# Performance work log

Hardware: AMD Instinct MI355X
Metric: run time of the kernel (lower is better)

The kernel has to match this reference:

```python
import jax, jax.numpy as jnp
import numpy as np

B, L, H, E, EH = 8, 96, 8, 64, 128

def setup_inputs() -> dict:
    key = jax.random.key(0)
    ks = jax.random.split(key, 5)
    x = jax.random.normal(ks[0], (B, L, H, E), jnp.float32)
    # strictly increasing, distinct time points (required by the past/future split)
    gaps = jax.random.uniform(ks[1], (L,), jnp.float32, 0.01, 0.1)
    timeslot = jnp.cumsum(gaps)
    W1 = jax.random.normal(ks[2], (E, EH), jnp.float32) / np.sqrt(E).astype(np.float32)
    b1 = jnp.zeros((EH,), jnp.float32)
    W2 = jax.random.normal(ks[3], (EH, E), jnp.float32) / np.sqrt(EH).astype(np.float32)
    b2 = jnp.zeros((E,), jnp.float32)
    return dict(x=x, timeslot=timeslot, W1=W1, b1=b1, W2=W2, b2=b2)

def reference(x, timeslot, W1, b1, W2, b2):
    Bd, Ld, Hd, Ed = x.shape

    def f(t, y):  # neural odefunc: MLP over feature dim E (t unused by the MLP)
        return jnp.tanh(y @ W1 + b1) @ W2 + b2

    def rk4_step(y, t0, dt):  # torchdiffeq 'rk4' = 3/8-rule RK4, one step per grid interval
        k1 = f(t0, y)
        k2 = f(t0 + dt / 3, y + dt * k1 / 3)
        k3 = f(t0 + 2 * dt / 3, y + dt * (k2 - k1 / 3))
        k4 = f(t0 + dt, y + dt * (k1 - k2 + k3))
        return y + dt * (k1 + 3 * (k2 + k3) + k4) / 8

    # Per-index initial states: S0[idx] = x[:, idx] flattened to (B*H, E)
    S0 = jnp.transpose(x, (1, 0, 2, 3)).reshape(Ld, Bd * Hd, Ed)
    idxs = jnp.arange(Ld)

    # Forward integration: state for index idx is advanced over t_s -> t_{s+1} once s >= idx.
    def fwd_step(S, s):
        t0 = timeslot[s]
        dt = timeslot[s + 1] - t0
        S2 = rk4_step(S, t0, dt)
        S = jnp.where((idxs <= s)[:, None, None], S2, S)
        return S, S  # emitted state corresponds to time t_{s+1}

    _, ys_f = jax.lax.scan(fwd_step, S0, jnp.arange(Ld - 1))
    z_fwd = jnp.concatenate([S0[None], ys_f], axis=0)  # [L_j, L_idx, B*H, E]

    # Backward integration: state for idx is advanced over t_s -> t_{s-1} once s <= idx.
    def bwd_step(S, s):
        t0 = timeslot[s]
        dt = timeslot[s - 1] - t0  # negative
        S2 = rk4_step(S, t0, dt)
        S = jnp.where((idxs >= s)[:, None, None], S2, S)
        return S, S  # emitted state corresponds to time t_{s-1}

    _, ys_b = jax.lax.scan(bwd_step, S0, jnp.arange(Ld - 1, 0, -1))
    z_bwd = jnp.concatenate([jnp.flip(ys_b, axis=0), S0[None]], axis=0)  # [L_j, L_idx, B*H, E]

    jj = jnp.arange(Ld)[:, None]
    z = jnp.where((jj >= idxs[None, :])[:, :, None, None], z_fwd, z_bwd)
    z = z.reshape(Ld, Ld, Bd, Hd, Ed)          # [L_j, L_idx, B, H, E]
    x1 = jnp.transpose(z, (2, 1, 0, 3, 4))      # [B, L_idx, L_j, H, E]
    x0 = jnp.broadcast_to(x[:, :, None], (Bd, Ld, Ld, Hd, Ed))
    return jnp.stack([x0, x1], axis=-1)          # [B, L, L, H, E, 2]
```

## Files before the change

kernel.cpp:

```cpp
#include <hip/hip_runtime.h>
#include <stdint.h>

#define Lc 96
#define Hc 8
#define Ec 64
#define EHc 128
#define APu 72
#define HPu 136
#define JS (Hc * Ec * 2)

typedef __attribute__((ext_vector_type(8))) short short8;
typedef __attribute__((ext_vector_type(4))) float floatx4;

union FragH { uint16_t h[8]; short8 v; };

__device__ __forceinline__ float fast_tanh(float x) {
    const float e = __builtin_amdgcn_exp2f(x * 2.8853900817779268f);
    return 1.0f - 2.0f * __builtin_amdgcn_rcpf(e + 1.0f);
}

__device__ __forceinline__ void lds_barrier() {
    asm volatile("s_waitcnt lgkmcnt(0)\n\ts_barrier" ::: "memory");
}

__global__ __launch_bounds__(256, 2)
void ode_mfma_kernel(const float* __restrict__ x, const float* __restrict__ ts,
                     const float* __restrict__ W1, const float* __restrict__ b1,
                     const float* __restrict__ W2, const float* __restrict__ b2,
                     float* __restrict__ out)
{
    __shared__ alignas(16) uint16_t A_hi[16 * APu];
    __shared__ alignas(16) uint16_t A_lo[16 * APu];
    __shared__ alignas(16) uint16_t H_hi[16 * HPu];
    __shared__ alignas(16) uint16_t H_lo[16 * HPu];
    __shared__ float tss[Lc];

    const int tid  = threadIdx.x;
    const int w    = tid >> 6;
    const int lane = tid & 63;
    const int g    = lane >> 4;
    const int c    = lane & 15;

    if (tid < Lc) tss[tid] = ts[tid];

    short8 w1h[2][2], w1l[2][2];
#pragma unroll
    for (int ct = 0; ct < 2; ++ct)
#pragma unroll
        for (int ks = 0; ks < 2; ++ks) {
            FragH fh, fl;
#pragma unroll
            for (int j = 0; j < 8; ++j) {
                const int k = ks * 32 + g * 8 + j;
                const int n = 32 * w + 16 * ct + c;
                const float v = W1[k * EHc + n];
                const uint32_t uv = __float_as_uint(v);
                const float hf = __uint_as_float(uv & 0xffff0000u);
                fh.h[j] = (uint16_t)(uv >> 16);
                fl.h[j] = (uint16_t)(__float_as_uint(v - hf) >> 16);
            }
            w1h[ct][ks] = fh.v; w1l[ct][ks] = fl.v;
        }
    short8 w2h[4], w2l[4];
#pragma unroll
    for (int ks = 0; ks < 4; ++ks) {
        FragH fh, fl;
#pragma unroll
        for (int j = 0; j < 8; ++j) {
            const int k = ks * 32 + g * 8 + j;
            const int n = 16 * w + c;
            const float v = W2[k * Ec + n];
            const uint32_t uv = __float_as_uint(v);
            const float hf = __uint_as_float(uv & 0xffff0000u);
            fh.h[j] = (uint16_t)(uv >> 16);
            fl.h[j] = (uint16_t)(__float_as_uint(v - hf) >> 16);
        }
        w2h[ks] = fh.v; w2l[ks] = fl.v;
    }

    const float b1v0 = b1[32 * w + c];
    const float b1v1 = b1[32 * w + 16 + c];
    const float b2v  = b2[16 * w + c];

    const int t_blk = (blockIdx.x * 16) >> 6;
    const int fs    = (Lc - 1) - t_blk;
    const int col   = 16 * w + c;

    float y0_[4], y_[4];
    float* outp[4];
#pragma unroll
    for (int reg = 0; reg < 4; ++reg) {
        const int rs = blockIdx.x * 16 + g * 4 + reg;
        const int bidx = (rs & 63) >> 3;
        const int hh   = rs & 7;
        const float v0 = x[((bidx * Lc + t_blk) * Hc + hh) * Ec + col];
        y0_[reg] = v0; y_[reg] = v0;
        outp[reg] = out + (size_t)(bidx * Lc + t_blk) * (Lc * JS) + hh * (Ec * 2) + col * 2;
        float2 o; o.x = v0; o.y = v0;
        *(float2*)(outp[reg] + (size_t)t_blk * JS) = o;
        const int r = g * 4 + reg;
        const uint32_t uv = __float_as_uint(v0);
        A_hi[r * APu + col] = (uint16_t)(uv >> 16);
        A_lo[r * APu + col] =
            (uint16_t)(__float_as_uint(v0 - __uint_as_float(uv & 0xffff0000u)) >> 16);
    }
    __syncthreads();

    const int arow = c * APu + g * 8;
    const int hrow = c * HPu + g * 8;
    const int hcol = 32 * w + c;

    auto evalf = [&]() -> floatx4 {
        const short8 a0h = *(const short8*)(A_hi + arow);
        const short8 a1h = *(const short8*)(A_hi + arow + 32);
        const short8 a0l = *(const short8*)(A_lo + arow);
        const short8 a1l = *(const short8*)(A_lo + arow + 32);

        floatx4 p0 = {b1v0, b1v0, b1v0, b1v0};
        floatx4 p1 = {b1v1, b1v1, b1v1, b1v1};
        p0 = __builtin_amdgcn_mfma_f32_16x16x32_bf16(a0h, w1h[0][0], p0, 0, 0, 0);
        p0 = __builtin_amdgcn_mfma_f32_16x16x32_bf16(a0h, w1l[0][0], p0, 0, 0, 0);
        p0 = __builtin_amdgcn_mfma_f32_16x16x32_bf16(a0l, w1h[0][0], p0, 0, 0, 0);
        p1 = __builtin_amdgcn_mfma_f32_16x16x32_bf16(a0h, w1h[1][0], p1, 0, 0, 0);
        p1 = __builtin_amdgcn_mfma_f32_16x16x32_bf16(a0h, w1l[1][0], p1, 0, 0, 0);
        p1 = __builtin_amdgcn_mfma_f32_16x16x32_bf16(a0l, w1h[1][0], p1, 0, 0, 0);
        p0 = __builtin_amdgcn_mfma_f32_16x16x32_bf16(a1h, w1h[0][1], p0, 0, 0, 0);
        p0 = __builtin_amdgcn_mfma_f32_16x16x32_bf16(a1h, w1l[0][1], p0, 0, 0, 0);
        p0 = __builtin_amdgcn_mfma_f32_16x16x32_bf16(a1l, w1h[0][1], p0, 0, 0, 0);
        p1 = __builtin_amdgcn_mfma_f32_16x16x32_bf16(a1h, w1h[1][1], p1, 0, 0, 0);
        p1 = __builtin_amdgcn_mfma_f32_16x16x32_bf16(a1h, w1l[1][1], p1, 0, 0, 0);
        p1 = __builtin_amdgcn_mfma_f32_16x16x32_bf16(a1l, w1h[1][1], p1, 0, 0, 0);

#pragma unroll
        for (int reg = 0; reg < 4; ++reg) {
            const int r = g * 4 + reg;
            const float t0 = fast_tanh(p0[reg]);
            const float t1 = fast_tanh(p1[reg]);
            const uint32_t u0 = __float_as_uint(t0);
            const uint32_t u1 = __float_as_uint(t1);
            H_hi[r * HPu + hcol]      = (uint16_t)(u0 >> 16);
            H_lo[r * HPu + hcol]      =
                (uint16_t)(__float_as_uint(t0 - __uint_as_float(u0 & 0xffff0000u)) >> 16);
            H_hi[r * HPu + hcol + 16] = (uint16_t)(u1 >> 16);
            H_lo[r * HPu + hcol + 16] =
                (uint16_t)(__float_as_uint(t1 - __uint_as_float(u1 & 0xffff0000u)) >> 16);
        }
        lds_barrier();

        floatx4 o = {b2v, b2v, b2v, b2v};
#pragma unroll
        for (int ks = 0; ks < 4; ++ks) {
            const short8 hh_ = *(const short8*)(H_hi + hrow + ks * 32);
            const short8 hl_ = *(const short8*)(H_lo + hrow + ks * 32);
            o = __builtin_amdgcn_mfma_f32_16x16x32_bf16(hh_, w2h[ks], o, 0, 0, 0);
            o = __builtin_amdgcn_mfma_f32_16x16x32_bf16(hh_, w2l[ks], o, 0, 0, 0);
            o = __builtin_amdgcn_mfma_f32_16x16x32_bf16(hl_, w2h[ks], o, 0, 0, 0);
        }
        return o;
    };

    auto putA = [&](const float* a4) {
#pragma unroll
        for (int reg = 0; reg < 4; ++reg) {
            const int r = g * 4 + reg;
            const float v = a4[reg];
            const uint32_t uv = __float_as_uint(v);
            A_hi[r * APu + col] = (uint16_t)(uv >> 16);
            A_lo[r * APu + col] =
                (uint16_t)(__float_as_uint(v - __uint_as_float(uv & 0xffff0000u)) >> 16);
        }
        lds_barrier();
    };

    for (int v = 0; v < Lc - 1; ++v) {
        float dt; int jo;
        if (v < fs) { const int s = t_blk + v;        dt = tss[s + 1] - tss[s]; jo = s + 1; }
        else        { const int s = t_blk - (v - fs); dt = tss[s - 1] - tss[s]; jo = s - 1; }

        float a[4];
        const floatx4 k1 = evalf();
#pragma unroll
        for (int reg = 0; reg < 4; ++reg)
            a[reg] = fmaf(dt * (1.0f / 3.0f), k1[reg], y_[reg]);
        putA(a);
        const floatx4 k2 = evalf();
#pragma unroll
        for (int reg = 0; reg < 4; ++reg)
            a[reg] = y_[reg] + dt * (k2[reg] - (1.0f / 3.0f) * k1[reg]);
        putA(a);
        const floatx4 k3 = evalf();
#pragma unroll
        for (int reg = 0; reg < 4; ++reg)
            a[reg] = y_[reg] + dt * (k1[reg] - k2[reg] + k3[reg]);
        putA(a);
        const floatx4 k4 = evalf();
#pragma unroll
        for (int reg = 0; reg < 4; ++reg) {
            y_[reg] += dt * (k1[reg] + 3.0f * (k2[reg] + k3[reg]) + k4[reg]) * 0.125f;
            float2 o; o.x = y0_[reg]; o.y = y_[reg];
            *(float2*)(outp[reg] + (size_t)jo * JS) = o;
        }
        if (v + 1 == fs) {
#pragma unroll
            for (int reg = 0; reg < 4; ++reg) y_[reg] = y0_[reg];
        }
#pragma unroll
        for (int reg = 0; reg < 4; ++reg) a[reg] = y_[reg];
        putA(a);
    }
}

extern "C" void kernel_launch(void* const* d_in, const int* in_sizes, int n_in,
                              void* d_out, int out_size, void* d_ws, size_t ws_size,
                              hipStream_t stream) {
    const float* x  = (const float*)d_in[0];
    const float* ts = (const float*)d_in[1];
    const float* W1 = (const float*)d_in[2];
    const float* b1 = (const float*)d_in[3];
    const float* W2 = (const float*)d_in[4];
    const float* b2 = (const float*)d_in[5];
    float* out = (float*)d_out;

    dim3 grid(6144 / 16);
    dim3 block(256);
    ode_mfma_kernel<<<grid, block, 0, stream>>>(x, ts, W1, b1, W2, b2, out);
}
```

Measured before the change: 625.6 us.

## Halve block to two waves, each computing double output tiles per RK stage

The block drops from four wavefronts to two. Each wave now handles four hidden-column tiles in the first MLP layer and two output-column tiles in the second, with the weight fragments for both kept in registers. This halves the number of waves that meet at each of the many LDS barriers per RK step and gives each wave more independent MFMA chains, including split accumulators in the second layer. The cost is more serial work per wave and higher register pressure, and with 384 blocks of two waves there is less parallelism per CU to hide latency.

```diff
diff --git a/kernel.cpp b/kernel.cpp
--- a/kernel.cpp
+++ b/kernel.cpp
@@ -23,7 +23,11 @@
     asm volatile("s_waitcnt lgkmcnt(0)\n\ts_barrier" ::: "memory");
 }
 
-__global__ __launch_bounds__(256, 2)
+#define MF(acc, A, B) acc = __builtin_amdgcn_mfma_f32_16x16x32_bf16((A), (B), (acc), 0, 0, 0)
+
+struct Pair { floatx4 o0, o1; };
+
+__global__ __launch_bounds__(128, 1)
 void ode_mfma_kernel(const float* __restrict__ x, const float* __restrict__ ts,
                      const float* __restrict__ W1, const float* __restrict__ b1,
                      const float* __restrict__ W2, const float* __restrict__ b2,
@@ -43,16 +47,16 @@
 
     if (tid < Lc) tss[tid] = ts[tid];
 
-    short8 w1h[2][2], w1l[2][2];
-#pragma unroll
-    for (int ct = 0; ct < 2; ++ct)
+    short8 w1h[4][2], w1l[4][2];
+#pragma unroll
+    for (int ct = 0; ct < 4; ++ct)
 #pragma unroll
         for (int ks = 0; ks < 2; ++ks) {
             FragH fh, fl;
 #pragma unroll
             for (int j = 0; j < 8; ++j) {
                 const int k = ks * 32 + g * 8 + j;
-                const int n = 32 * w + 16 * ct + c;
+                const int n = 64 * w + 16 * ct + c;
                 const float v = W1[k * EHc + n];
                 const uint32_t uv = __float_as_uint(v);
                 const float hf = __uint_as_float(uv & 0xffff0000u);
@@ -61,114 +65,122 @@
             }
             w1h[ct][ks] = fh.v; w1l[ct][ks] = fl.v;
         }
-    short8 w2h[4], w2l[4];
-#pragma unroll
-    for (int ks = 0; ks < 4; ++ks) {
-        FragH fh, fl;
-#pragma unroll
-        for (int j = 0; j < 8; ++j) {
-            const int k = ks * 32 + g * 8 + j;
-            const int n = 16 * w + c;
-            const float v = W2[k * Ec + n];
-            const uint32_t uv = __float_as_uint(v);
-            const float hf = __uint_as_float(uv & 0xffff0000u);
-            fh.h[j] = (uint16_t)(uv >> 16);
-            fl.h[j] = (uint16_t)(__float_as_uint(v - hf) >> 16);
-        }
-        w2h[ks] = fh.v; w2l[ks] = fl.v;
-    }
-
-    const float b1v0 = b1[32 * w + c];
-    const float b1v1 = b1[32 * w + 16 + c];
-    const float b2v  = b2[16 * w + c];
+    short8 w2h[2][4], w2l[2][4];
+#pragma unroll
+    for (int nt = 0; nt < 2; ++nt)
+#pragma unroll
+        for (int ks = 0; ks < 4; ++ks) {
+            FragH fh, fl;
+#pragma unroll
+            for (int j = 0; j < 8; ++j) {
+                const int k = ks * 32 + g * 8 + j;
+                const int n = 32 * w + 16 * nt + c;
+                const float v = W2[k * Ec + n];
+                const uint32_t uv = __float_as_uint(v);
+                const float hf = __uint_as_float(uv & 0xffff0000u);
+                fh.h[j] = (uint16_t)(uv >> 16);
+                fl.h[j] = (uint16_t)(__float_as_uint(v - hf) >> 16);
+            }
+            w2h[nt][ks] = fh.v; w2l[nt][ks] = fl.v;
+        }
+
+    float b1v[4], b2v[2];
+#pragma unroll
+    for (int ct = 0; ct < 4; ++ct) b1v[ct] = b1[64 * w + 16 * ct + c];
+#pragma unroll
+    for (int nt = 0; nt < 2; ++nt) b2v[nt] = b2[32 * w + 16 * nt + c];
 
     const int t_blk = (blockIdx.x * 16) >> 6;
     const int fs    = (Lc - 1) - t_blk;
-    const int col   = 16 * w + c;
-
-    float y0_[4], y_[4];
-    float* outp[4];
+    const int col0  = 32 * w + c;
+
+    float y0_[2][4], y_[2][4];
+    float* outR[4];
 #pragma unroll
     for (int reg = 0; reg < 4; ++reg) {
         const int rs = blockIdx.x * 16 + g * 4 + reg;
         const int bidx = (rs & 63) >> 3;
         const int hh   = rs & 7;
-        const float v0 = x[((bidx * Lc + t_blk) * Hc + hh) * Ec + col];
-        y0_[reg] = v0; y_[reg] = v0;
-        outp[reg] = out + (size_t)(bidx * Lc + t_blk) * (Lc * JS) + hh * (Ec * 2) + col * 2;
-        float2 o; o.x = v0; o.y = v0;
-        *(float2*)(outp[reg] + (size_t)t_blk * JS) = o;
+        outR[reg] = out + (size_t)(bidx * Lc + t_blk) * (Lc * JS) + hh * (Ec * 2) + col0 * 2;
         const int r = g * 4 + reg;
-        const uint32_t uv = __float_as_uint(v0);
-        A_hi[r * APu + col] = (uint16_t)(uv >> 16);
-        A_lo[r * APu + col] =
-            (uint16_t)(__float_as_uint(v0 - __uint_as_float(uv & 0xffff0000u)) >> 16);
+#pragma unroll
+        for (int nt = 0; nt < 2; ++nt) {
+            const float v0 = x[((bidx * Lc + t_blk) * Hc + hh) * Ec + col0 + 16 * nt];
+            y0_[nt][reg] = v0; y_[nt][reg] = v0;
+            float2 o; o.x = v0; o.y = v0;
+            *(float2*)(outR[reg] + (size_t)t_blk * JS + nt * 32) = o;
+            const uint32_t uv = __float_as_uint(v0);
+            A_hi[r * APu + col0 + 16 * nt] = (uint16_t)(uv >> 16);
+            A_lo[r * APu + col0 + 16 * nt] =
+                (uint16_t)(__float_as_uint(v0 - __uint_as_float(uv & 0xffff0000u)) >> 16);
+        }
     }
     __syncthreads();
 
     const int arow = c * APu + g * 8;
     const int hrow = c * HPu + g * 8;
-    const int hcol = 32 * w + c;
-
-    auto evalf = [&]() -> floatx4 {
-        const short8 a0h = *(const short8*)(A_hi + arow);
-        const short8 a1h = *(const short8*)(A_hi + arow + 32);
-        const short8 a0l = *(const short8*)(A_lo + arow);
-        const short8 a1l = *(const short8*)(A_lo + arow + 32);
-
-        floatx4 p0 = {b1v0, b1v0, b1v0, b1v0};
-        floatx4 p1 = {b1v1, b1v1, b1v1, b1v1};
-        p0 = __builtin_amdgcn_mfma_f32_16x16x32_bf16(a0h, w1h[0][0], p0, 0, 0, 0);
-        p0 = __builtin_amdgcn_mfma_f32_16x16x32_bf16(a0h, w1l[0][0], p0, 0, 0, 0);
-        p0 = __builtin_amdgcn_mfma_f32_16x16x32_bf16(a0l, w1h[0][0], p0, 0, 0, 0);
-        p1 = __builtin_amdgcn_mfma_f32_16x16x32_bf16(a0h, w1h[1][0], p1, 0, 0, 0);
-        p1 = __builtin_amdgcn_mfma_f32_16x16x32_bf16(a0h, w1l[1][0], p1, 0, 0, 0);
-        p1 = __builtin_amdgcn_mfma_f32_16x16x32_bf16(a0l, w1h[1][0], p1, 0, 0, 0);
-        p0 = __builtin_amdgcn_mfma_f32_16x16x32_bf16(a1h, w1h[0][1], p0, 0, 0, 0);
-        p0 = __builtin_amdgcn_mfma_f32_16x16x32_bf16(a1h, w1l[0][1], p0, 0, 0, 0);
-        p0 = __builtin_amdgcn_mfma_f32_16x16x32_bf16(a1l, w1h[0][1], p0, 0, 0, 0);
-        p1 = __builtin_amdgcn_mfma_f32_16x16x32_bf16(a1h, w1h[1][1], p1, 0, 0, 0);
-        p1 = __builtin_amdgcn_mfma_f32_16x16x32_bf16(a1h, w1l[1][1], p1, 0, 0, 0);
-        p1 = __builtin_amdgcn_mfma_f32_16x16x32_bf16(a1l, w1h[1][1], p1, 0, 0, 0);
-
-#pragma unroll
-        for (int reg = 0; reg < 4; ++reg) {
-            const int r = g * 4 + reg;
-            const float t0 = fast_tanh(p0[reg]);
-            const float t1 = fast_tanh(p1[reg]);
-            const uint32_t u0 = __float_as_uint(t0);
-            const uint32_t u1 = __float_as_uint(t1);
-            H_hi[r * HPu + hcol]      = (uint16_t)(u0 >> 16);
-            H_lo[r * HPu + hcol]      =
-                (uint16_t)(__float_as_uint(t0 - __uint_as_float(u0 & 0xffff0000u)) >> 16);
-            H_hi[r * HPu + hcol + 16] = (uint16_t)(u1 >> 16);
-            H_lo[r * HPu + hcol + 16] =
-                (uint16_t)(__float_as_uint(t1 - __uint_as_float(u1 & 0xffff0000u)) >> 16);
+
+    auto evalf = [&]() -> Pair {
+        short8 ah[2], al[2];
+        ah[0] = *(const short8*)(A_hi + arow);
+        ah[1] = *(const short8*)(A_hi + arow + 32);
+        al[0] = *(const short8*)(A_lo + arow);
+        al[1] = *(const short8*)(A_lo + arow + 32);
+
+        floatx4 p[4];
+#pragma unroll
+        for (int ct = 0; ct < 4; ++ct) {
+            floatx4 acc = {b1v[ct], b1v[ct], b1v[ct], b1v[ct]};
+            MF(acc, ah[0], w1h[ct][0]); MF(acc, ah[0], w1l[ct][0]); MF(acc, al[0], w1h[ct][0]);
+            MF(acc, ah[1], w1h[ct][1]); MF(acc, ah[1], w1l[ct][1]); MF(acc, al[1], w1h[ct][1]);
+            p[ct] = acc;
+        }
+
+#pragma unroll
+        for (int ct = 0; ct < 4; ++ct) {
+#pragma unroll
+            for (int reg = 0; reg < 4; ++reg) {
+                const int r = g * 4 + reg;
+                const float t0 = fast_tanh(p[ct][reg]);
+                const uint32_t u0 = __float_as_uint(t0);
+                H_hi[r * HPu + 64 * w + 16 * ct + c] = (uint16_t)(u0 >> 16);
+                H_lo[r * HPu + 64 * w + 16 * ct + c] =
+                    (uint16_t)(__float_as_uint(t0 - __uint_as_float(u0 & 0xffff0000u)) >> 16);
+            }
         }
         lds_barrier();
 
-        floatx4 o = {b2v, b2v, b2v, b2v};
+        const floatx4 z = {0.f, 0.f, 0.f, 0.f};
+        floatx4 o0a = {b2v[0], b2v[0], b2v[0], b2v[0]}, o0b = z;
+        floatx4 o1a = {b2v[1], b2v[1], b2v[1], b2v[1]}, o1b = z;
 #pragma unroll
         for (int ks = 0; ks < 4; ++ks) {
             const short8 hh_ = *(const short8*)(H_hi + hrow + ks * 32);
             const short8 hl_ = *(const short8*)(H_lo + hrow + ks * 32);
-            o = __builtin_amdgcn_mfma_f32_16x16x32_bf16(hh_, w2h[ks], o, 0, 0, 0);
-            o = __builtin_amdgcn_mfma_f32_16x16x32_bf16(hh_, w2l[ks], o, 0, 0, 0);
-            o = __builtin_amdgcn_mfma_f32_16x16x32_bf16(hl_, w2h[ks], o, 0, 0, 0);
-        }
-        return o;
+            if (ks & 1) {
+                MF(o0b, hh_, w2h[0][ks]); MF(o0b, hh_, w2l[0][ks]); MF(o0b, hl_, w2h[0][ks]);
+                MF(o1b, hh_, w2h[1][ks]); MF(o1b, hh_, w2l[1][ks]); MF(o1b, hl_, w2h[1][ks]);
+            } else {
+                MF(o0a, hh_, w2h[0][ks]); MF(o0a, hh_, w2l[0][ks]); MF(o0a, hl_, w2h[0][ks]);
+                MF(o1a, hh_, w2h[1][ks]); MF(o1a, hh_, w2l[1][ks]); MF(o1a, hl_, w2h[1][ks]);
+            }
+        }
+        Pair r; r.o0 = o0a + o0b; r.o1 = o1a + o1b;
+        return r;
     };
 
-    auto putA = [&](const float* a4) {
-#pragma unroll
-        for (int reg = 0; reg < 4; ++reg) {
-            const int r = g * 4 + reg;
-            const float v = a4[reg];
-            const uint32_t uv = __float_as_uint(v);
-            A_hi[r * APu + col] = (uint16_t)(uv >> 16);
-            A_lo[r * APu + col] =
-                (uint16_t)(__float_as_uint(v - __uint_as_float(uv & 0xffff0000u)) >> 16);
-        }
+    auto putA = [&](const float (&a)[2][4]) {
+#pragma unroll
+        for (int nt = 0; nt < 2; ++nt)
+#pragma unroll
+            for (int reg = 0; reg < 4; ++reg) {
+                const int r = g * 4 + reg;
+                const float v = a[nt][reg];
+                const uint32_t uv = __float_as_uint(v);
+                A_hi[r * APu + col0 + 16 * nt] = (uint16_t)(uv >> 16);
+                A_lo[r * APu + col0 + 16 * nt] =
+                    (uint16_t)(__float_as_uint(v - __uint_as_float(uv & 0xffff0000u)) >> 16);
+            }
         lds_barrier();
     };
 
@@ -177,35 +189,60 @@
         if (v < fs) { const int s = t_blk + v;        dt = tss[s + 1] - tss[s]; jo = s + 1; }
         else        { const int s = t_blk - (v - fs); dt = tss[s - 1] - tss[s]; jo = s - 1; }
 
-        float a[4];
-        const floatx4 k1 = evalf();
-#pragma unroll
-        for (int reg = 0; reg < 4; ++reg)
-            a[reg] = fmaf(dt * (1.0f / 3.0f), k1[reg], y_[reg]);
-        putA(a);
-        const floatx4 k2 = evalf();
-#pragma unroll
-        for (int reg = 0; reg < 4; ++reg)
-            a[reg] = y_[reg] + dt * (k2[reg] - (1.0f / 3.0f) * k1[reg]);
-        putA(a);
-        const floatx4 k3 = evalf();
-#pragma unroll
-        for (int reg = 0; reg < 4; ++reg)
-            a[reg] = y_[reg] + dt * (k1[reg] - k2[reg] + k3[reg]);
-        putA(a);
-        const floatx4 k4 = evalf();
-#pragma unroll
-        for (int reg = 0; reg < 4; ++reg) {
-            y_[reg] += dt * (k1[reg] + 3.0f * (k2[reg] + k3[reg]) + k4[reg]) * 0.125f;
-            float2 o; o.x = y0_[reg]; o.y = y_[reg];
-            *(float2*)(outp[reg] + (size_t)jo * JS) = o;
+        float a[2][4], k1[2][4], k2[2][4], k3[2][4];
+
+        const Pair r1 = evalf();
+#pragma unroll
+        for (int reg = 0; reg < 4; ++reg) {
+            k1[0][reg] = r1.o0[reg]; k1[1][reg] = r1.o1[reg];
+#pragma unroll
+            for (int nt = 0; nt < 2; ++nt)
+                a[nt][reg] = fmaf(dt * (1.0f / 3.0f), k1[nt][reg], y_[nt][reg]);
+        }
+        putA(a);
+
+        const Pair r2 = evalf();
+#pragma unroll
+        for (int reg = 0; reg < 4; ++reg) {
+            k2[0][reg] = r2.o0[reg]; k2[1][reg] = r2.o1[reg];
+#pragma unroll
+            for (int nt = 0; nt < 2; ++nt)
+                a[nt][reg] = y_[nt][reg] + dt * (k2[nt][reg] - (1.0f / 3.0f) * k1[nt][reg]);
+        }
+        putA(a);
+
+        const Pair r3 = evalf();
+#pragma unroll
+        for (int reg = 0; reg < 4; ++reg) {
+            k3[0][reg] = r3.o0[reg]; k3[1][reg] = r3.o1[reg];
+#pragma unroll
+            for (int nt = 0; nt < 2; ++nt)
+                a[nt][reg] = y_[nt][reg] + dt * (k1[nt][reg] - k2[nt][reg] + k3[nt][reg]);
+        }
+        putA(a);
+
+        const Pair r4 = evalf();
+#pragma unroll
+        for (int reg = 0; reg < 4; ++reg) {
+            const float k4_0 = r4.o0[reg], k4_1 = r4.o1[reg];
+            y_[0][reg] += dt * (k1[0][reg] + 3.0f * (k2[0][reg] + k3[0][reg]) + k4_0) * 0.125f;
+            y_[1][reg] += dt * (k1[1][reg] + 3.0f * (k2[1][reg] + k3[1][reg]) + k4_1) * 0.125f;
+#pragma unroll
+            for (int nt = 0; nt < 2; ++nt) {
+                float2 o; o.x = y0_[nt][reg]; o.y = y_[nt][reg];
+                *(float2*)(outR[reg] + (size_t)jo * JS + nt * 32) = o;
+            }
         }
         if (v + 1 == fs) {
 #pragma unroll
-            for (int reg = 0; reg < 4; ++reg) y_[reg] = y0_[reg];
-        }
-#pragma unroll
-        for (int reg = 0; reg < 4; ++reg) a[reg] = y_[reg];
+            for (int nt = 0; nt < 2; ++nt)
+#pragma unroll
+                for (int reg = 0; reg < 4; ++reg) y_[nt][reg] = y0_[nt][reg];
+        }
+#pragma unroll
+        for (int nt = 0; nt < 2; ++nt)
+#pragma unroll
+            for (int reg = 0; reg < 4; ++reg) a[nt][reg] = y_[nt][reg];
         putA(a);
     }
 }
@@ -222,6 +259,6 @@
     float* out = (float*)d_out;
 
     dim3 grid(6144 / 16);
-    dim3 block(256);
+    dim3 block(128);
     ode_mfma_kernel<<<grid, block, 0, stream>>>(x, ts, W1, b1, W2, b2, out);
 }
```

After: 694.7 us. 1.11x slower.

## Split forward and backward integration into separate blocks and break MFMA dependency chains

Applied to the files above, without the earlier changes.

Each 16-row tile is now handled by two blocks, one integrating forward and one backward, which halves the serial chain length per block and doubles the grid to 768 blocks. Blocks with no steps exit early after writing the diagonal element. The MFMA accumulations are split into independent accumulators summed at the end to shorten dependency chains, and s_setprio wraps the MFMA bursts. The cost is extra weight-fragment setup per block, and per-block work becomes uneven.

```diff
diff --git a/kernel.cpp b/kernel.cpp
--- a/kernel.cpp
+++ b/kernel.cpp
@@ -22,6 +22,8 @@
 __device__ __forceinline__ void lds_barrier() {
     asm volatile("s_waitcnt lgkmcnt(0)\n\ts_barrier" ::: "memory");
 }
+
+#define MF(acc, A, B) acc = __builtin_amdgcn_mfma_f32_16x16x32_bf16((A), (B), (acc), 0, 0, 0)
 
 __global__ __launch_bounds__(256, 2)
 void ode_mfma_kernel(const float* __restrict__ x, const float* __restrict__ ts,
@@ -41,6 +43,29 @@
     const int g    = lane >> 4;
     const int c    = lane & 15;
 
+    const int tile  = blockIdx.x >> 1;
+    const int dir   = blockIdx.x & 1;
+    const int t_blk = tile >> 2;
+    const int nv    = dir ? t_blk : (Lc - 1 - t_blk);
+    const int col   = 16 * w + c;
+
+    float y0_[4], y_[4];
+    float* outp[4];
+#pragma unroll
+    for (int reg = 0; reg < 4; ++reg) {
+        const int rs = tile * 16 + g * 4 + reg;
+        const int bidx = (rs & 63) >> 3;
+        const int hh   = rs & 7;
+        const float v0 = x[((bidx * Lc + t_blk) * Hc + hh) * Ec + col];
+        y0_[reg] = v0; y_[reg] = v0;
+        outp[reg] = out + (size_t)(bidx * Lc + t_blk) * (Lc * JS) + hh * (Ec * 2) + col * 2;
+        if (dir == 0) {
+            float2 o; o.x = v0; o.y = v0;
+            *(float2*)(outp[reg] + (size_t)t_blk * JS) = o;
+        }
+    }
+    if (nv == 0) return;
+
     if (tid < Lc) tss[tid] = ts[tid];
 
     short8 w1h[2][2], w1l[2][2];
@@ -82,23 +107,10 @@
     const float b1v1 = b1[32 * w + 16 + c];
     const float b2v  = b2[16 * w + c];
 
-    const int t_blk = (blockIdx.x * 16) >> 6;
-    const int fs    = (Lc - 1) - t_blk;
-    const int col   = 16 * w + c;
-
-    float y0_[4], y_[4];
-    float* outp[4];
 #pragma unroll
     for (int reg = 0; reg < 4; ++reg) {
-        const int rs = blockIdx.x * 16 + g * 4 + reg;
-        const int bidx = (rs & 63) >> 3;
-        const int hh   = rs & 7;
-        const float v0 = x[((bidx * Lc + t_blk) * Hc + hh) * Ec + col];
-        y0_[reg] = v0; y_[reg] = v0;
-        outp[reg] = out + (size_t)(bidx * Lc + t_blk) * (Lc * JS) + hh * (Ec * 2) + col * 2;
-        float2 o; o.x = v0; o.y = v0;
-        *(float2*)(outp[reg] + (size_t)t_blk * JS) = o;
         const int r = g * 4 + reg;
+        const float v0 = y0_[reg];
         const uint32_t uv = __float_as_uint(v0);
         A_hi[r * APu + col] = (uint16_t)(uv >> 16);
         A_lo[r * APu + col] =
@@ -116,20 +128,17 @@
         const short8 a0l = *(const short8*)(A_lo + arow);
         const short8 a1l = *(const short8*)(A_lo + arow + 32);
 
-        floatx4 p0 = {b1v0, b1v0, b1v0, b1v0};
-        floatx4 p1 = {b1v1, b1v1, b1v1, b1v1};
-        p0 = __builtin_amdgcn_mfma_f32_16x16x32_bf16(a0h, w1h[0][0], p0, 0, 0, 0);
-        p0 = __builtin_amdgcn_mfma_f32_16x16x32_bf16(a0h, w1l[0][0], p0, 0, 0, 0);
-        p0 = __builtin_amdgcn_mfma_f32_16x16x32_bf16(a0l, w1h[0][0], p0, 0, 0, 0);
-        p1 = __builtin_amdgcn_mfma_f32_16x16x32_bf16(a0h, w1h[1][0], p1, 0, 0, 0);
-        p1 = __builtin_amdgcn_mfma_f32_16x16x32_bf16(a0h, w1l[1][0], p1, 0, 0, 0);
-        p1 = __builtin_amdgcn_mfma_f32_16x16x32_bf16(a0l, w1h[1][0], p1, 0, 0, 0);
-        p0 = __builtin_amdgcn_mfma_f32_16x16x32_bf16(a1h, w1h[0][1], p0, 0, 0, 0);
-        p0 = __builtin_amdgcn_mfma_f32_16x16x32_bf16(a1h, w1l[0][1], p0, 0, 0, 0);
-        p0 = __builtin_amdgcn_mfma_f32_16x16x32_bf16(a1l, w1h[0][1], p0, 0, 0, 0);
-        p1 = __builtin_amdgcn_mfma_f32_16x16x32_bf16(a1h, w1h[1][1], p1, 0, 0, 0);
-        p1 = __builtin_amdgcn_mfma_f32_16x16x32_bf16(a1h, w1l[1][1], p1, 0, 0, 0);
-        p1 = __builtin_amdgcn_mfma_f32_16x16x32_bf16(a1l, w1h[1][1], p1, 0, 0, 0);
+        const floatx4 z = {0.f, 0.f, 0.f, 0.f};
+        floatx4 p0a = {b1v0, b1v0, b1v0, b1v0}, p0b = z;
+        floatx4 p1a = {b1v1, b1v1, b1v1, b1v1}, p1b = z;
+        __builtin_amdgcn_s_setprio(1);
+        MF(p0a, a0h, w1h[0][0]); MF(p0a, a0h, w1l[0][0]); MF(p0a, a0l, w1h[0][0]);
+        MF(p1a, a0h, w1h[1][0]); MF(p1a, a0h, w1l[1][0]); MF(p1a, a0l, w1h[1][0]);
+        MF(p0b, a1h, w1h[0][1]); MF(p0b, a1h, w1l[0][1]); MF(p0b, a1l, w1h[0][1]);
+        MF(p1b, a1h, w1h[1][1]); MF(p1b, a1h, w1l[1][1]); MF(p1b, a1l, w1h[1][1]);
+        __builtin_amdgcn_s_setprio(0);
+        const floatx4 p0 = p0a + p0b;
+        const floatx4 p1 = p1a + p1b;
 
 #pragma unroll
         for (int reg = 0; reg < 4; ++reg) {
@@ -147,16 +156,22 @@
         }
         lds_barrier();
 
-        floatx4 o = {b2v, b2v, b2v, b2v};
-#pragma unroll
-        for (int ks = 0; ks < 4; ++ks) {
-            const short8 hh_ = *(const short8*)(H_hi + hrow + ks * 32);
-            const short8 hl_ = *(const short8*)(H_lo + hrow + ks * 32);
-            o = __builtin_amdgcn_mfma_f32_16x16x32_bf16(hh_, w2h[ks], o, 0, 0, 0);
-            o = __builtin_amdgcn_mfma_f32_16x16x32_bf16(hh_, w2l[ks], o, 0, 0, 0);
-            o = __builtin_amdgcn_mfma_f32_16x16x32_bf16(hl_, w2h[ks], o, 0, 0, 0);
-        }
-        return o;
+        floatx4 oa = {b2v, b2v, b2v, b2v}, ob = z, oc = z, od = z;
+        const short8 h0 = *(const short8*)(H_hi + hrow);
+        const short8 l0 = *(const short8*)(H_lo + hrow);
+        const short8 h1 = *(const short8*)(H_hi + hrow + 32);
+        const short8 l1 = *(const short8*)(H_lo + hrow + 32);
+        const short8 h2 = *(const short8*)(H_hi + hrow + 64);
+        const short8 l2 = *(const short8*)(H_lo + hrow + 64);
+        const short8 h3 = *(const short8*)(H_hi + hrow + 96);
+        const short8 l3 = *(const short8*)(H_lo + hrow + 96);
+        __builtin_amdgcn_s_setprio(1);
+        MF(oa, h0, w2h[0]); MF(oa, h0, w2l[0]); MF(oa, l0, w2h[0]);
+        MF(ob, h1, w2h[1]); MF(ob, h1, w2l[1]); MF(ob, l1, w2h[1]);
+        MF(oc, h2, w2h[2]); MF(oc, h2, w2l[2]); MF(oc, l2, w2h[2]);
+        MF(od, h3, w2h[3]); MF(od, h3, w2l[3]); MF(od, l3, w2h[3]);
+        __builtin_amdgcn_s_setprio(0);
+        return (oa + ob) + (oc + od);
     };
 
     auto putA = [&](const float* a4) {
@@ -172,10 +187,11 @@
         lds_barrier();
     };
 
-    for (int v = 0; v < Lc - 1; ++v) {
-        float dt; int jo;
-        if (v < fs) { const int s = t_blk + v;        dt = tss[s + 1] - tss[s]; jo = s + 1; }
-        else        { const int s = t_blk - (v - fs); dt = tss[s - 1] - tss[s]; jo = s - 1; }
+    for (int v = 0; v < nv; ++v) {
+        int s, jo;
+        if (dir == 0) { s = t_blk + v; jo = s + 1; }
+        else          { s = t_blk - v; jo = s - 1; }
+        const float dt = tss[jo] - tss[s];
 
         float a[4];
         const floatx4 k1 = evalf();
@@ -199,10 +215,6 @@
             y_[reg] += dt * (k1[reg] + 3.0f * (k2[reg] + k3[reg]) + k4[reg]) * 0.125f;
             float2 o; o.x = y0_[reg]; o.y = y_[reg];
             *(float2*)(outp[reg] + (size_t)jo * JS) = o;
-        }
-        if (v + 1 == fs) {
-#pragma unroll
-            for (int reg = 0; reg < 4; ++reg) y_[reg] = y0_[reg];
         }
 #pragma unroll
         for (int reg = 0; reg < 4; ++reg) a[reg] = y_[reg];
@@ -221,7 +233,7 @@
     const float* b2 = (const float*)d_in[5];
     float* out = (float*)d_out;
 
-    dim3 grid(6144 / 16);
+    dim3 grid(768);
     dim3 block(256);
     ode_mfma_kernel<<<grid, block, 0, stream>>>(x, ts, W1, b1, W2, b2, out);
 }
```

Result: slower. 649.7 us (+3.9%).
